# Kernel optimization log

Hardware: AMD Instinct MI355X
Metric: run time of the kernel (lower is better)

## Reference

```python
import jax, jax.numpy as jnp
import numpy as np

B, C, Hd, Wd = 8, 256, 64, 64
NUM_HEAD = 4
RATIO = 0.25
OUT_CH = int(NUM_HEAD * C * RATIO)      # 256
HEAD_DIM = OUT_CH // NUM_HEAD           # 64
EPS = 1e-5


def conv1x1(x, w, b=None):
    # x: [B,Ci,H,W], w: [Co,Ci]
    y = jnp.einsum('bchw,oc->bohw', x, w)
    if b is not None:
        y = y + b[None, :, None, None]
    return y


def setup_inputs() -> dict:
    key = jax.random.key(0)
    ks = jax.random.split(key, 16)
    s = lambda fan: 1.0 / np.sqrt(fan)
    return {
        'key':   jax.random.normal(ks[0], (B, C, Hd, Wd), jnp.float32),
        'query': jax.random.normal(ks[1], (B, C, Hd, Wd), jnp.float32),
        'wq': jax.random.normal(ks[2], (OUT_CH, C), jnp.float32) * s(C),
        'bq': jax.random.normal(ks[3], (OUT_CH,), jnp.float32) * 0.01,
        'wk': jax.random.normal(ks[4], (OUT_CH, C), jnp.float32) * s(C),
        'bk': jax.random.normal(ks[5], (OUT_CH,), jnp.float32) * 0.01,
        'wv': jax.random.normal(ks[6], (OUT_CH, C), jnp.float32) * s(C),
        'bv': jax.random.normal(ks[7], (OUT_CH,), jnp.float32) * 0.01,
        'wW': jax.random.normal(ks[8], (C, HEAD_DIM), jnp.float32) * s(HEAD_DIM),
        'bn_gamma': jnp.ones((C,), jnp.float32),
        'bn_beta': jnp.zeros((C,), jnp.float32),
        'bn_mean': jax.random.normal(ks[9], (C,), jnp.float32) * 0.1,
        'bn_var': jax.random.uniform(ks[10], (C,), jnp.float32, 0.5, 1.5),
        'w3': jax.random.normal(ks[11], (C, 2 * C, 3, 3), jnp.float32) * s(2 * C * 9),
        'b3': jax.random.normal(ks[12], (C,), jnp.float32) * 0.01,
        'w1': jax.random.normal(ks[13], (C, C), jnp.float32) * s(C),
        'b1': jax.random.normal(ks[14], (C,), jnp.float32) * 0.01,
    }


def reference(key, query, wq, bq, wk, bk, wv, bv, wW,
              bn_gamma, bn_beta, bn_mean, bn_var, w3, b3, w1, b1):
    b, c, h, w = query.shape
    q = conv1x1(query, wq, bq).reshape(b, NUM_HEAD, HEAD_DIM, h, w)
    k = conv1x1(key, wk, bk).reshape(b, NUM_HEAD, HEAD_DIM, h, w)
    v = conv1x1(key, wv, bv).reshape(b, NUM_HEAD, HEAD_DIM, h, w)

    att = (q * k).sum(axis=2) / np.sqrt(OUT_CH)          # [b, num_head, h, w]
    sm = jax.nn.softmax(att, axis=1)[:, :, None]         # softmax over heads
    weighted = (v * sm).sum(axis=1)                      # [b, head_dim, h, w]

    # W: 1x1 conv (no bias) + BatchNorm (inference)
    out = conv1x1(weighted, wW)
    inv = bn_gamma / jnp.sqrt(bn_var + EPS)
    out = out * inv[None, :, None, None] + (bn_beta - bn_mean * inv)[None, :, None, None]

    # fuse: ConvBlock (reflect-pad 3x3 conv + ELU) then 1x1 conv
    x = jnp.concatenate([key, out], axis=1)              # [b, 2C, h, w]
    x = jnp.pad(x, ((0, 0), (0, 0), (1, 1), (1, 1)), mode='reflect')
    x = jax.lax.conv_general_dilated(x, w3, (1, 1), 'VALID',
                                     dimension_numbers=('NCHW', 'OIHW', 'NCHW'))
    x = jax.nn.elu(x + b3[None, :, None, None])
    return conv1x1(x, w1, b1)
```

## Files before the change

### kernel.cpp

```cpp
#include <hip/hip_runtime.h>
#include <hip/hip_bf16.h>

typedef unsigned short u16;
typedef unsigned int u32;
typedef short bf16x8 __attribute__((ext_vector_type(8)));
typedef float f32x4 __attribute__((ext_vector_type(4)));

#define NPX 32768

__device__ __forceinline__ u16 f2bf(float f) {
  union { float f; u32 u; } v; v.f = f;
  return (u16)((v.u + 0x7FFFu + ((v.u >> 16) & 1u)) >> 16);
}

__device__ __forceinline__ void gload16(const u16* g, u16* l) {
  __builtin_amdgcn_global_load_lds(
      (const __attribute__((address_space(1))) void*)g,
      (__attribute__((address_space(3))) void*)l, 16, 0, 0);
}


__global__ __launch_bounds__(256) void prep_small(
    const float* __restrict__ wq, const float* __restrict__ wk,
    const float* __restrict__ wv, const float* __restrict__ w1,
    const float* __restrict__ wW, const float* __restrict__ gamma,
    const float* __restrict__ beta, const float* __restrict__ mean,
    const float* __restrict__ var,
    u16* __restrict__ wqb, u16* __restrict__ wkb, u16* __restrict__ wvb,
    u16* __restrict__ w1b, u16* __restrict__ wWpb, float* __restrict__ bWp) {
  int idx = blockIdx.x * 256 + threadIdx.x;
  if (idx < 65536) {
    int o = idx >> 8, c = idx & 255;
    int dst = (c >> 5) * 8192 + o * 32 + ((c >> 3) & 3) * 8 + (c & 7);
    wqb[dst] = f2bf(wq[idx]);
    wkb[dst] = f2bf(wk[idx]);
    wvb[dst] = f2bf(wv[idx]);
    w1b[dst] = f2bf(w1[idx]);
  } else if (idx < 65536 + 16384) {
    int j = idx - 65536;
    int o = j >> 6, c = j & 63;
    float inv = gamma[o] * rsqrtf(var[o] + 1e-5f);
    int dst = (c >> 5) * 8192 + o * 32 + ((c >> 3) & 3) * 8 + (c & 7);
    wWpb[dst] = f2bf(wW[j] * inv);
  } else if (idx < 65536 + 16384 + 256) {
    int o = idx - 65536 - 16384;
    float inv = gamma[o] * rsqrtf(var[o] + 1e-5f);
    bWp[o] = beta[o] - mean[o] * inv;
  }
}

__global__ __launch_bounds__(256) void prep_w3t(const float* __restrict__ w3,
                                                u16* __restrict__ w3c) {
  int idx = blockIdx.x * 256 + threadIdx.x;
  int o = idx >> 9, c = idx & 511;
  int cb = c >> 6, ks = (c >> 5) & 1, lk = (c >> 3) & 3, e = c & 7;
  #pragma unroll
  for (int t = 0; t < 9; ++t)
    w3c[(size_t)(((t * 8 + cb) * 2 + ks) * 256 + o) * 32 + lk * 8 + e] =
        f2bf(w3[idx * 9 + t]);
}

__global__ __launch_bounds__(256, 2) void attn_kernel(
    const float* __restrict__ qsrc, const float* __restrict__ ksrc,
    u16* __restrict__ xcat,
    const u16* __restrict__ wqb, const u16* __restrict__ wkb, const u16* __restrict__ wvb,
    const float* __restrict__ bq, const float* __restrict__ bk, const float* __restrict__ bv,
    const u16* __restrict__ wWpb, const float* __restrict__ bWp) {
  __shared__ __align__(16) char smem[74752];
  u16* aq = (u16*)smem;
  u16* ak = (u16*)(smem + 32768);
  u16* tile = (u16*)(smem + 65536);
  float* att_s = (float*)(smem + 65536);
  u16* wsum = (u16*)(smem + 66560);
  float* wbuf = (float*)smem;
  u16* ob = (u16*)smem;

  int tid = threadIdx.x;
  int lane = tid & 63, wv_ = tid >> 6;
  int lc = lane & 15, lk = lane >> 4;
  int px0 = blockIdx.x * 64;
  int b = px0 >> 12, hw0 = px0 & 4095;

  #pragma unroll
  for (int t = 0; t < 8; ++t) {
    const float* src = (t < 4) ? qsrc : ksrc;
    int cc = t & 3;
    #pragma unroll
    for (int i = 0; i < 4; ++i) {
      int idx = tid + 256 * i;
      int c = idx >> 4, p4 = idx & 15;
      const float4 v = *(const float4*)&src[(size_t)(b * 256 + cc * 64 + c) * 4096 + hw0 + p4 * 4];
      u32 lo = f2bf(v.x) | ((u32)f2bf(v.y) << 16);
      u32 hi = f2bf(v.z) | ((u32)f2bf(v.w) << 16);
      *(uint2*)&tile[c * 72 + p4 * 4] = make_uint2(lo, hi);
    }
    __syncthreads();
    int px = tid >> 2, cq = tid & 3;
    u32 vv[8];
    #pragma unroll
    for (int i = 0; i < 8; ++i) {
      u16 a = tile[(cq * 16 + 2 * i) * 72 + px];
      u16 bb = tile[(cq * 16 + 2 * i + 1) * 72 + px];
      vv[i] = a | ((u32)bb << 16);
    }
    u16* dstl = (t < 4) ? aq : ak;
    int c8 = cc * 8 + cq * 2;
    *(uint4*)(dstl + px * 256 + (c8 ^ (px & 7)) * 8) = make_uint4(vv[0], vv[1], vv[2], vv[3]);
    *(uint4*)(dstl + px * 256 + ((c8 + 1) ^ (px & 7)) * 8) = make_uint4(vv[4], vv[5], vv[6], vv[7]);
    if (t >= 4) {
      u16* dp = xcat + (size_t)(px0 + px) * 512 + cc * 64 + cq * 16;
      *(uint4*)dp = make_uint4(vv[0], vv[1], vv[2], vv[3]);
      *(uint4*)(dp + 8) = make_uint4(vv[4], vv[5], vv[6], vv[7]);
    }
    __syncthreads();
  }

  f32x4 zero4 = {0.f, 0.f, 0.f, 0.f};
  f32x4 accq[4][4], acck[4][4];
  #pragma unroll
  for (int mi = 0; mi < 4; ++mi)
    #pragma unroll
    for (int nj = 0; nj < 4; ++nj) { accq[mi][nj] = zero4; acck[mi][nj] = zero4; }

  #pragma unroll
  for (int kk = 0; kk < 8; ++kk) {
    bf16x8 afq[4], afk[4], bfq[4], bfk[4];
    #pragma unroll
    for (int mi = 0; mi < 4; ++mi) {
      int px = mi * 16 + lc;
      int s = (kk * 4 + lk) ^ (px & 7);
      afq[mi] = *(const bf16x8*)(aq + px * 256 + s * 8);
      afk[mi] = *(const bf16x8*)(ak + px * 256 + s * 8);
    }
    #pragma unroll
    for (int nj = 0; nj < 4; ++nj) {
      int n = wv_ * 64 + nj * 16 + lc;
      bfq[nj] = *(const bf16x8*)(wqb + kk * 8192 + n * 32 + lk * 8);
      bfk[nj] = *(const bf16x8*)(wkb + kk * 8192 + n * 32 + lk * 8);
    }
    #pragma unroll
    for (int mi = 0; mi < 4; ++mi)
      #pragma unroll
      for (int nj = 0; nj < 4; ++nj) {
        accq[mi][nj] = __builtin_amdgcn_mfma_f32_16x16x32_bf16(afq[mi], bfq[nj], accq[mi][nj], 0, 0, 0);
        acck[mi][nj] = __builtin_amdgcn_mfma_f32_16x16x32_bf16(afk[mi], bfk[nj], acck[mi][nj], 0, 0, 0);
      }
  }

  #pragma unroll
  for (int nj = 0; nj < 4; ++nj) {
    float bqv = bq[wv_ * 64 + nj * 16 + lc];
    float bkv = bk[wv_ * 64 + nj * 16 + lc];
    #pragma unroll
    for (int mi = 0; mi < 4; ++mi)
      #pragma unroll
      for (int j = 0; j < 4; ++j) { accq[mi][nj][j] += bqv; acck[mi][nj][j] += bkv; }
  }

  float smx[4][4];
  #pragma unroll
  for (int mi = 0; mi < 4; ++mi)
    #pragma unroll
    for (int j = 0; j < 4; ++j) {
      float p = 0.f;
      #pragma unroll
      for (int nj = 0; nj < 4; ++nj) p += accq[mi][nj][j] * acck[mi][nj][j];
      p += __shfl_xor(p, 1);
      p += __shfl_xor(p, 2);
      p += __shfl_xor(p, 4);
      p += __shfl_xor(p, 8);
      float a = p * 0.0625f;
      smx[mi][j] = a;
      if (lc == 0) att_s[wv_ * 64 + mi * 16 + lk * 4 + j] = a;
    }
  __syncthreads();
  #pragma unroll
  for (int mi = 0; mi < 4; ++mi)
    #pragma unroll
    for (int j = 0; j < 4; ++j) {
      int px = mi * 16 + lk * 4 + j;
      float a0 = att_s[px], a1 = att_s[64 + px], a2 = att_s[128 + px], a3 = att_s[192 + px];
      float mx = fmaxf(fmaxf(a0, a1), fmaxf(a2, a3));
      float e0 = __expf(a0 - mx), e1 = __expf(a1 - mx);
      float e2 = __expf(a2 - mx), e3 = __expf(a3 - mx);
      float den = e0 + e1 + e2 + e3;
      float ew = wv_ == 0 ? e0 : (wv_ == 1 ? e1 : (wv_ == 2 ? e2 : e3));
      smx[mi][j] = ew / den;
    }

  f32x4 accv[4][4];
  #pragma unroll
  for (int mi = 0; mi < 4; ++mi)
    #pragma unroll
    for (int nj = 0; nj < 4; ++nj) accv[mi][nj] = zero4;
  #pragma unroll
  for (int kk = 0; kk < 8; ++kk) {
    bf16x8 af[4], bfr[4];
    #pragma unroll
    for (int mi = 0; mi < 4; ++mi) {
      int px = mi * 16 + lc;
      int s = (kk * 4 + lk) ^ (px & 7);
      af[mi] = *(const bf16x8*)(ak + px * 256 + s * 8);
    }
    #pragma unroll
    for (int nj = 0; nj < 4; ++nj) {
      int n = wv_ * 64 + nj * 16 + lc;
      bfr[nj] = *(const bf16x8*)(wvb + kk * 8192 + n * 32 + lk * 8);
    }
    #pragma unroll
    for (int mi = 0; mi < 4; ++mi)
      #pragma unroll
      for (int nj = 0; nj < 4; ++nj)
        accv[mi][nj] = __builtin_amdgcn_mfma_f32_16x16x32_bf16(af[mi], bfr[nj], accv[mi][nj], 0, 0, 0);
  }
  #pragma unroll
  for (int nj = 0; nj < 4; ++nj) {
    float bvv = bv[wv_ * 64 + nj * 16 + lc];
    #pragma unroll
    for (int mi = 0; mi < 4; ++mi)
      #pragma unroll
      for (int j = 0; j < 4; ++j) accv[mi][nj][j] += bvv;
  }
  __syncthreads();

  #pragma unroll
  for (int mi = 0; mi < 4; ++mi)
    #pragma unroll
    for (int nj = 0; nj < 4; ++nj)
      #pragma unroll
      for (int j = 0; j < 4; ++j) {
        int px = mi * 16 + lk * 4 + j;
        wbuf[(wv_ * 64 + px) * 64 + nj * 16 + lc] = smx[mi][j] * accv[mi][nj][j];
      }
  __syncthreads();

  #pragma unroll
  for (int i = 0; i < 2; ++i) {
    int idx = tid + 256 * i;
    int px = idx >> 3, c = idx & 7;
    float a8[8] = {0.f, 0.f, 0.f, 0.f, 0.f, 0.f, 0.f, 0.f};
    #pragma unroll
    for (int h = 0; h < 4; ++h) {
      const float4* p = (const float4*)(wbuf + ((h * 64 + px) * 64 + c * 8));
      float4 u0 = p[0], u1 = p[1];
      a8[0] += u0.x; a8[1] += u0.y; a8[2] += u0.z; a8[3] += u0.w;
      a8[4] += u1.x; a8[5] += u1.y; a8[6] += u1.z; a8[7] += u1.w;
    }
    u32 p0 = f2bf(a8[0]) | ((u32)f2bf(a8[1]) << 16);
    u32 p1 = f2bf(a8[2]) | ((u32)f2bf(a8[3]) << 16);
    u32 p2 = f2bf(a8[4]) | ((u32)f2bf(a8[5]) << 16);
    u32 p3 = f2bf(a8[6]) | ((u32)f2bf(a8[7]) << 16);
    *(uint4*)(wsum + px * 64 + (c ^ (px & 7)) * 8) = make_uint4(p0, p1, p2, p3);
  }
  __syncthreads();

  f32x4 a4[4][4];
  #pragma unroll
  for (int mi = 0; mi < 4; ++mi)
    #pragma unroll
    for (int nj = 0; nj < 4; ++nj) a4[mi][nj] = zero4;
  #pragma unroll
  for (int kk = 0; kk < 2; ++kk) {
    bf16x8 af[4], bfr[4];
    #pragma unroll
    for (int mi = 0; mi < 4; ++mi) {
      int px = mi * 16 + lc;
      int s = (kk * 4 + lk) ^ (px & 7);
      af[mi] = *(const bf16x8*)(wsum + px * 64 + s * 8);
    }
    #pragma unroll
    for (int nj = 0; nj < 4; ++nj) {
      int n = wv_ * 64 + nj * 16 + lc;
      bfr[nj] = *(const bf16x8*)(wWpb + kk * 8192 + n * 32 + lk * 8);
    }
    #pragma unroll
    for (int mi = 0; mi < 4; ++mi)
      #pragma unroll
      for (int nj = 0; nj < 4; ++nj)
        a4[mi][nj] = __builtin_amdgcn_mfma_f32_16x16x32_bf16(af[mi], bfr[nj], a4[mi][nj], 0, 0, 0);
  }
  #pragma unroll
  for (int nj = 0; nj < 4; ++nj) {
    int o = wv_ * 64 + nj * 16 + lc;
    float bb = bWp[o];
    #pragma unroll
    for (int mi = 0; mi < 4; ++mi)
      #pragma unroll
      for (int j = 0; j < 4; ++j) {
        int px = mi * 16 + lk * 4 + j;
        ob[px * 264 + o] = f2bf(a4[mi][nj][j] + bb);
      }
  }
  __syncthreads();
  #pragma unroll
  for (int i = 0; i < 8; ++i) {
    int idx = tid + 256 * i;
    int px = idx >> 5, c8 = idx & 31;
    *(uint4*)(xcat + (size_t)(px0 + px) * 512 + 256 + c8 * 8) =
        *(const uint4*)(ob + px * 264 + c8 * 8);
  }
}

__global__ __launch_bounds__(512, 2) void conv3_kernel(
    const u16* __restrict__ xcat, const u16* __restrict__ w3c,
    const float* __restrict__ b3, const u16* __restrict__ w1b,
    const float* __restrict__ b1, float* __restrict__ out) {
  extern __shared__ __align__(16) u16 smem[];
  u16* xb0 = smem;
  u16* xb1 = smem + 16896;
  u16* wb0 = smem + 33792;
  u16* wb1 = smem + 50176;

  int tid = threadIdx.x;
  int lane = tid & 63, wave = tid >> 6;
  int lc = lane & 15, lk = lane >> 4;
  int wr = wave >> 2, wc = wave & 3;
  int b = blockIdx.x >> 5, r0 = (blockIdx.x & 31) * 2;

  int gx[4], gxt;
  #pragma unroll
  for (int i = 0; i < 5; ++i) {
    int idx = (i < 4) ? (tid + i * 512) : (2048 + lane);
    int px = idx >> 3, t = idx & 7;
    int row = px / 66;
    int pxr = px - row * 66;
    int h_in = r0 - 1 + row; h_in = h_in < 0 ? 1 : (h_in > 63 ? 62 : h_in);
    int w_in = pxr - 1;      w_in = w_in < 0 ? 1 : (w_in > 63 ? 62 : w_in);
    int g = ((b * 64 + h_in) * 64 + w_in) * 512 + (t ^ (pxr & 7)) * 8;
    if (i < 4) gx[i] = g; else gxt = g;
  }
  int gw[4];
  #pragma unroll
  for (int i = 0; i < 4; ++i) {
    int p = tid + i * 512;
    int j = p ^ ((p >> 3) & 7);
    gw[i] = j * 8;
  }

#define STAGE_X(dst, cb_)                                                      \
  do {                                                                         \
    _Pragma("unroll") for (int i = 0; i < 4; ++i)                              \
        gload16(xcat + gx[i] + (cb_) * 64, (dst) + (size_t)(tid + i * 512) * 8); \
    if (wave == 0) gload16(xcat + gxt + (cb_) * 64, (dst) + (size_t)(2048 + lane) * 8); \
  } while (0)

#define STAGE_W(dst, slab)                                                     \
  do {                                                                         \
    const u16* wsrc = w3c + (size_t)(slab) * 16384;                            \
    _Pragma("unroll") for (int i = 0; i < 4; ++i)                              \
        gload16(wsrc + gw[i], (dst) + (size_t)(tid + i * 512) * 8);            \
  } while (0)

  f32x4 zero4 = {0.f, 0.f, 0.f, 0.f};
  f32x4 acc[4][4];
  #pragma unroll
  for (int mi = 0; mi < 4; ++mi)
    #pragma unroll
    for (int nj = 0; nj < 4; ++nj) acc[mi][nj] = zero4;

  STAGE_X(xb0, 0);
  STAGE_W(wb0, 0);
  __syncthreads();

  for (int cb = 0; cb < 8; ++cb) {
    const u16* xcur = (cb & 1) ? xb1 : xb0;
    #pragma unroll
    for (int tap = 0; tap < 9; ++tap) {
      const u16* wcur = ((cb + tap) & 1) ? wb1 : wb0;
      u16* wnxt = ((cb + tap) & 1) ? wb0 : wb1;
      if (tap < 8) {
        STAGE_W(wnxt, (tap + 1) * 8 + cb);
      } else if (cb < 7) {
        STAGE_W(wnxt, cb + 1);
        STAGE_X((cb & 1) ? xb0 : xb1, cb + 1);
      }
      const int dy = tap / 3, dx = tap % 3;
      #pragma unroll
      for (int ks = 0; ks < 2; ++ks) {
        bf16x8 af[4], bfr[4];
        #pragma unroll
        for (int mi = 0; mi < 4; ++mi) {
          int pp = mi * 16 + lc + dx;
          af[mi] = *(const bf16x8*)(xcur + ((wr + dy) * 66 + pp) * 64 +
                                    (((ks * 4 + lk) ^ (pp & 7)) * 8));
        }
        #pragma unroll
        for (int nj = 0; nj < 4; ++nj) {
          int n = wc * 64 + nj * 16 + lc;
          int j = ks * 1024 + n * 4 + lk;
          int p = j ^ ((j >> 3) & 7);
          bfr[nj] = *(const bf16x8*)(wcur + p * 8);
        }
        __builtin_amdgcn_s_setprio(1);
        #pragma unroll
        for (int mi = 0; mi < 4; ++mi)
          #pragma unroll
          for (int nj = 0; nj < 4; ++nj)
            acc[mi][nj] = __builtin_amdgcn_mfma_f32_16x16x32_bf16(
                af[mi], bfr[nj], acc[mi][nj], 0, 0, 0);
        __builtin_amdgcn_s_setprio(0);
      }
      __syncthreads();
    }
  }
#undef STAGE_X
#undef STAGE_W

  u16* eb = smem;
  #pragma unroll
  for (int nj = 0; nj < 4; ++nj) {
    int o = wc * 64 + nj * 16 + lc;
    float bias = b3[o];
    #pragma unroll
    for (int mi = 0; mi < 4; ++mi)
      #pragma unroll
      for (int j = 0; j < 4; ++j) {
        int p = wr * 64 + mi * 16 + lk * 4 + j;
        float v = acc[mi][nj][j] + bias;
        v = v > 0.f ? v : (__expf(v) - 1.f);
        eb[p * 264 + o] = f2bf(v);
      }
  }
  __syncthreads();

  f32x4 acc2[4][4];
  #pragma unroll
  for (int mi = 0; mi < 4; ++mi)
    #pragma unroll
    for (int nj = 0; nj < 4; ++nj) acc2[mi][nj] = zero4;
  #pragma unroll
  for (int kk = 0; kk < 8; ++kk) {
    bf16x8 af[4], bfr[4];
    #pragma unroll
    for (int mi = 0; mi < 4; ++mi)
      af[mi] = *(const bf16x8*)(eb + (wr * 64 + mi * 16 + lc) * 264 + kk * 32 + lk * 8);
    #pragma unroll
    for (int nj = 0; nj < 4; ++nj)
      bfr[nj] = *(const bf16x8*)(w1b + kk * 8192 + (wc * 64 + nj * 16 + lc) * 32 + lk * 8);
    #pragma unroll
    for (int mi = 0; mi < 4; ++mi)
      #pragma unroll
      for (int nj = 0; nj < 4; ++nj)
        acc2[mi][nj] = __builtin_amdgcn_mfma_f32_16x16x32_bf16(af[mi], bfr[nj], acc2[mi][nj], 0, 0, 0);
  }
  #pragma unroll
  for (int nj = 0; nj < 4; ++nj) {
    int o = wc * 64 + nj * 16 + lc;
    float bias = b1[o];
    #pragma unroll
    for (int mi = 0; mi < 4; ++mi) {
      float4 v;
      v.x = acc2[mi][nj][0] + bias;
      v.y = acc2[mi][nj][1] + bias;
      v.z = acc2[mi][nj][2] + bias;
      v.w = acc2[mi][nj][3] + bias;
      *(float4*)&out[(size_t)(b * 256 + o) * 4096 + (r0 + wr) * 64 + mi * 16 + lk * 4] = v;
    }
  }
}

extern "C" void kernel_launch(void* const* d_in, const int* in_sizes, int n_in,
                              void* d_out, int out_size, void* d_ws, size_t ws_size,
                              hipStream_t stream) {
  const float* key   = (const float*)d_in[0];
  const float* query = (const float*)d_in[1];
  const float* wq    = (const float*)d_in[2];
  const float* bq    = (const float*)d_in[3];
  const float* wk    = (const float*)d_in[4];
  const float* bk    = (const float*)d_in[5];
  const float* wv    = (const float*)d_in[6];
  const float* bv    = (const float*)d_in[7];
  const float* wW    = (const float*)d_in[8];
  const float* gamma = (const float*)d_in[9];
  const float* beta  = (const float*)d_in[10];
  const float* mean  = (const float*)d_in[11];
  const float* var   = (const float*)d_in[12];
  const float* w3    = (const float*)d_in[13];
  const float* b3    = (const float*)d_in[14];
  const float* w1    = (const float*)d_in[15];
  const float* b1    = (const float*)d_in[16];
  float* out = (float*)d_out;

  char* ws = (char*)d_ws;
  u16* xcat  = (u16*)(ws + 16777216);
  u16* w3t   = (u16*)(ws + 67108864);
  u16* wqb   = (u16*)(ws + 69468160);
  u16* wkb   = (u16*)(ws + 69599232);
  u16* wvb   = (u16*)(ws + 69730304);
  u16* w1b   = (u16*)(ws + 69861376);
  u16* wWpb  = (u16*)(ws + 69992448);
  float* bWp = (float*)(ws + 70025216);

  (void)hipFuncSetAttribute((const void*)conv3_kernel,
                            hipFuncAttributeMaxDynamicSharedMemorySize, 133120);

  prep_small<<<321, 256, 0, stream>>>(wq, wk, wv, w1, wW, gamma, beta, mean, var,
                                      wqb, wkb, wvb, w1b, wWpb, bWp);
  prep_w3t<<<512, 256, 0, stream>>>(w3, w3t);
  attn_kernel<<<512, 256, 0, stream>>>(query, key, xcat, wqb, wkb, wvb,
                                       bq, bk, bv, wWpb, bWp);
  conv3_kernel<<<256, 512, 133120, stream>>>(xcat, w3t, b3, w1b, b1, out);
}
```

Before: 118.1 us.

## Shrink conv3 tiles to one output row and 32-channel K slabs for occupancy

The 3x3 conv kernel now has each block compute a single output row instead of two. It uses 32-channel K slabs instead of 64, which shrinks LDS from about 130KB of dynamic memory to about 58KB of static memory and allows more resident blocks per CU with twice as many blocks. The weight repack layout changes to match the new slab size, and block IDs are remapped so that consecutive blocks spread across batches. The trade-off is less reuse per staged tile, twice as many barrier-separated pipeline steps, and more halo reloading of input rows.

After: 134.3 us. +13.7%, slower.

```diff
diff --git a/kernel.cpp b/kernel.cpp
--- a/kernel.cpp
+++ b/kernel.cpp
@@ -53,10 +53,11 @@
                                                 u16* __restrict__ w3c) {
   int idx = blockIdx.x * 256 + threadIdx.x;
   int o = idx >> 9, c = idx & 511;
-  int cb = c >> 6, ks = (c >> 5) & 1, lk = (c >> 3) & 3, e = c & 7;
+  int cb = c >> 5, w = c & 31;
+  int lk = w >> 3, e = w & 7;
   #pragma unroll
   for (int t = 0; t < 9; ++t)
-    w3c[(size_t)(((t * 8 + cb) * 2 + ks) * 256 + o) * 32 + lk * 8 + e] =
+    w3c[(size_t)(t * 16 + cb) * 8192 + o * 32 + lk * 8 + e] =
         f2bf(w3[idx * 9 + t]);
 }
 
@@ -301,60 +302,60 @@
   }
 }
 
-__global__ __launch_bounds__(512, 2) void conv3_kernel(
+__global__ __launch_bounds__(512, 4) void conv3_kernel(
     const u16* __restrict__ xcat, const u16* __restrict__ w3c,
     const float* __restrict__ b3, const u16* __restrict__ w1b,
     const float* __restrict__ b1, float* __restrict__ out) {
-  extern __shared__ __align__(16) u16 smem[];
+  __shared__ __align__(16) u16 smem[29696];
   u16* xb0 = smem;
-  u16* xb1 = smem + 16896;
-  u16* wb0 = smem + 33792;
-  u16* wb1 = smem + 50176;
+  u16* xb1 = smem + 6656;
+  u16* wb0 = smem + 13312;
+  u16* wb1 = smem + 21504;
 
   int tid = threadIdx.x;
   int lane = tid & 63, wave = tid >> 6;
   int lc = lane & 15, lk = lane >> 4;
   int wr = wave >> 2, wc = wave & 3;
-  int b = blockIdx.x >> 5, r0 = (blockIdx.x & 31) * 2;
-
-  int gx[4], gxt;
-  #pragma unroll
-  for (int i = 0; i < 5; ++i) {
-    int idx = (i < 4) ? (tid + i * 512) : (2048 + lane);
-    int px = idx >> 3, t = idx & 7;
-    int row = px / 66;
-    int pxr = px - row * 66;
-    int h_in = r0 - 1 + row; h_in = h_in < 0 ? 1 : (h_in > 63 ? 62 : h_in);
-    int w_in = pxr - 1;      w_in = w_in < 0 ? 1 : (w_in > 63 ? 62 : w_in);
-    int g = ((b * 64 + h_in) * 64 + w_in) * 512 + (t ^ (pxr & 7)) * 8;
-    if (i < 4) gx[i] = g; else gxt = g;
-  }
-  int gw[4];
-  #pragma unroll
-  for (int i = 0; i < 4; ++i) {
-    int p = tid + i * 512;
-    int j = p ^ ((p >> 3) & 7);
-    gw[i] = j * 8;
-  }
-
-#define STAGE_X(dst, cb_)                                                      \
-  do {                                                                         \
-    _Pragma("unroll") for (int i = 0; i < 4; ++i)                              \
-        gload16(xcat + gx[i] + (cb_) * 64, (dst) + (size_t)(tid + i * 512) * 8); \
-    if (wave == 0) gload16(xcat + gxt + (cb_) * 64, (dst) + (size_t)(2048 + lane) * 8); \
+  int sbid = (blockIdx.x & 7) * 64 + (blockIdx.x >> 3);
+  int b = sbid >> 6, r = sbid & 63;
+
+  int gx0, gx1, gx2;
+  #pragma unroll
+  for (int i = 0; i < 3; ++i) {
+    int q = (i == 0) ? tid : (i == 1 ? 512 + tid : 768 + lane);
+    q = q < 792 ? q : 791;
+    int row = q / 264, rem = q - row * 264;
+    int s = rem / 66, px = rem - s * 66;
+    int h_in = r - 1 + row; h_in = h_in < 0 ? 1 : (h_in > 63 ? 62 : h_in);
+    int w_in = px - 1;      w_in = w_in < 0 ? 1 : (w_in > 63 ? 62 : w_in);
+    int g = ((b * 64 + h_in) * 64 + w_in) * 512 + s * 8;
+    if (i == 0) gx0 = g; else if (i == 1) gx1 = g; else gx2 = g;
+  }
+  int gw0, gw1;
+  {
+    int p0 = tid, p1 = tid + 512;
+    gw0 = (p0 ^ ((p0 >> 3) & 7)) * 8;
+    gw1 = (p1 ^ ((p1 >> 3) & 7)) * 8;
+  }
+
+#define STAGE_X(dst, cb_)                                                       \
+  do {                                                                          \
+    gload16(xcat + gx0 + (cb_) * 32, (dst) + (size_t)tid * 8);                  \
+    if (tid < 256) gload16(xcat + gx1 + (cb_) * 32, (dst) + (size_t)(512 + tid) * 8); \
+    if (wave == 0) gload16(xcat + gx2 + (cb_) * 32, (dst) + (size_t)(768 + lane) * 8); \
   } while (0)
 
-#define STAGE_W(dst, slab)                                                     \
-  do {                                                                         \
-    const u16* wsrc = w3c + (size_t)(slab) * 16384;                            \
-    _Pragma("unroll") for (int i = 0; i < 4; ++i)                              \
-        gload16(wsrc + gw[i], (dst) + (size_t)(tid + i * 512) * 8);            \
+#define STAGE_W(dst, slab)                                                      \
+  do {                                                                          \
+    const u16* wsrc = w3c + (size_t)(slab) * 8192;                              \
+    gload16(wsrc + gw0, (dst) + (size_t)tid * 8);                               \
+    gload16(wsrc + gw1, (dst) + (size_t)(tid + 512) * 8);                       \
   } while (0)
 
   f32x4 zero4 = {0.f, 0.f, 0.f, 0.f};
-  f32x4 acc[4][4];
-  #pragma unroll
-  for (int mi = 0; mi < 4; ++mi)
+  f32x4 acc[2][4];
+  #pragma unroll
+  for (int mi = 0; mi < 2; ++mi)
     #pragma unroll
     for (int nj = 0; nj < 4; ++nj) acc[mi][nj] = zero4;
 
@@ -362,44 +363,41 @@
   STAGE_W(wb0, 0);
   __syncthreads();
 
-  for (int cb = 0; cb < 8; ++cb) {
+  for (int cb = 0; cb < 16; ++cb) {
     const u16* xcur = (cb & 1) ? xb1 : xb0;
     #pragma unroll
     for (int tap = 0; tap < 9; ++tap) {
-      const u16* wcur = ((cb + tap) & 1) ? wb1 : wb0;
-      u16* wnxt = ((cb + tap) & 1) ? wb0 : wb1;
+      int par = (cb + tap) & 1;
+      const u16* wcur = par ? wb1 : wb0;
+      u16* wnxt = par ? wb0 : wb1;
       if (tap < 8) {
-        STAGE_W(wnxt, (tap + 1) * 8 + cb);
-      } else if (cb < 7) {
+        STAGE_W(wnxt, (tap + 1) * 16 + cb);
+      } else if (cb < 15) {
         STAGE_W(wnxt, cb + 1);
         STAGE_X((cb & 1) ? xb0 : xb1, cb + 1);
       }
       const int dy = tap / 3, dx = tap % 3;
-      #pragma unroll
-      for (int ks = 0; ks < 2; ++ks) {
-        bf16x8 af[4], bfr[4];
+      bf16x8 af[2], bfr[4];
+      #pragma unroll
+      for (int mi = 0; mi < 2; ++mi) {
+        int pp = wr * 32 + mi * 16 + lc + dx;
+        af[mi] = *(const bf16x8*)(xcur + ((dy * 4 + lk) * 66 + pp) * 8);
+      }
+      #pragma unroll
+      for (int nj = 0; nj < 4; ++nj) {
+        int n = wc * 64 + nj * 16 + lc;
+        int j = n * 4 + lk;
+        int p = j ^ ((j >> 3) & 7);
+        bfr[nj] = *(const bf16x8*)(wcur + p * 8);
+      }
+      __builtin_amdgcn_s_setprio(1);
+      #pragma unroll
+      for (int mi = 0; mi < 2; ++mi)
         #pragma unroll
-        for (int mi = 0; mi < 4; ++mi) {
-          int pp = mi * 16 + lc + dx;
-          af[mi] = *(const bf16x8*)(xcur + ((wr + dy) * 66 + pp) * 64 +
-                                    (((ks * 4 + lk) ^ (pp & 7)) * 8));
-        }
-        #pragma unroll
-        for (int nj = 0; nj < 4; ++nj) {
-          int n = wc * 64 + nj * 16 + lc;
-          int j = ks * 1024 + n * 4 + lk;
-          int p = j ^ ((j >> 3) & 7);
-          bfr[nj] = *(const bf16x8*)(wcur + p * 8);
-        }
-        __builtin_amdgcn_s_setprio(1);
-        #pragma unroll
-        for (int mi = 0; mi < 4; ++mi)
-          #pragma unroll
-          for (int nj = 0; nj < 4; ++nj)
-            acc[mi][nj] = __builtin_amdgcn_mfma_f32_16x16x32_bf16(
-                af[mi], bfr[nj], acc[mi][nj], 0, 0, 0);
-        __builtin_amdgcn_s_setprio(0);
-      }
+        for (int nj = 0; nj < 4; ++nj)
+          acc[mi][nj] = __builtin_amdgcn_mfma_f32_16x16x32_bf16(
+              af[mi], bfr[nj], acc[mi][nj], 0, 0, 0);
+      __builtin_amdgcn_s_setprio(0);
       __syncthreads();
     }
   }
@@ -412,33 +410,33 @@
     int o = wc * 64 + nj * 16 + lc;
     float bias = b3[o];
     #pragma unroll
-    for (int mi = 0; mi < 4; ++mi)
+    for (int mi = 0; mi < 2; ++mi)
       #pragma unroll
       for (int j = 0; j < 4; ++j) {
-        int p = wr * 64 + mi * 16 + lk * 4 + j;
+        int p = wr * 32 + mi * 16 + lk * 4 + j;
         float v = acc[mi][nj][j] + bias;
         v = v > 0.f ? v : (__expf(v) - 1.f);
-        eb[p * 264 + o] = f2bf(v);
-      }
-  }
-  __syncthreads();
-
-  f32x4 acc2[4][4];
-  #pragma unroll
-  for (int mi = 0; mi < 4; ++mi)
+        eb[p * 260 + o] = f2bf(v);
+      }
+  }
+  __syncthreads();
+
+  f32x4 acc2[2][4];
+  #pragma unroll
+  for (int mi = 0; mi < 2; ++mi)
     #pragma unroll
     for (int nj = 0; nj < 4; ++nj) acc2[mi][nj] = zero4;
   #pragma unroll
   for (int kk = 0; kk < 8; ++kk) {
-    bf16x8 af[4], bfr[4];
-    #pragma unroll
-    for (int mi = 0; mi < 4; ++mi)
-      af[mi] = *(const bf16x8*)(eb + (wr * 64 + mi * 16 + lc) * 264 + kk * 32 + lk * 8);
+    bf16x8 af[2], bfr[4];
+    #pragma unroll
+    for (int mi = 0; mi < 2; ++mi)
+      af[mi] = *(const bf16x8*)(eb + (wr * 32 + mi * 16 + lc) * 260 + kk * 32 + lk * 8);
     #pragma unroll
     for (int nj = 0; nj < 4; ++nj)
       bfr[nj] = *(const bf16x8*)(w1b + kk * 8192 + (wc * 64 + nj * 16 + lc) * 32 + lk * 8);
     #pragma unroll
-    for (int mi = 0; mi < 4; ++mi)
+    for (int mi = 0; mi < 2; ++mi)
       #pragma unroll
       for (int nj = 0; nj < 4; ++nj)
         acc2[mi][nj] = __builtin_amdgcn_mfma_f32_16x16x32_bf16(af[mi], bfr[nj], acc2[mi][nj], 0, 0, 0);
@@ -448,13 +446,13 @@
     int o = wc * 64 + nj * 16 + lc;
     float bias = b1[o];
     #pragma unroll
-    for (int mi = 0; mi < 4; ++mi) {
+    for (int mi = 0; mi < 2; ++mi) {
       float4 v;
       v.x = acc2[mi][nj][0] + bias;
       v.y = acc2[mi][nj][1] + bias;
       v.z = acc2[mi][nj][2] + bias;
       v.w = acc2[mi][nj][3] + bias;
-      *(float4*)&out[(size_t)(b * 256 + o) * 4096 + (r0 + wr) * 64 + mi * 16 + lk * 4] = v;
+      *(float4*)&out[(size_t)(b * 256 + o) * 4096 + r * 64 + wr * 32 + mi * 16 + lk * 4] = v;
     }
   }
 }
@@ -491,13 +489,10 @@
   u16* wWpb  = (u16*)(ws + 69992448);
   float* bWp = (float*)(ws + 70025216);
 
-  (void)hipFuncSetAttribute((const void*)conv3_kernel,
-                            hipFuncAttributeMaxDynamicSharedMemorySize, 133120);
-
   prep_small<<<321, 256, 0, stream>>>(wq, wk, wv, w1, wW, gamma, beta, mean, var,
                                       wqb, wkb, wvb, w1b, wWpb, bWp);
   prep_w3t<<<512, 256, 0, stream>>>(w3, w3t);
   attn_kernel<<<512, 256, 0, stream>>>(query, key, xcat, wqb, wkb, wvb,
                                        bq, bk, bv, wWpb, bWp);
-  conv3_kernel<<<256, 512, 133120, stream>>>(xcat, w3t, b3, w1b, b1, out);
-}
+  conv3_kernel<<<512, 512, 0, stream>>>(xcat, w3t, b3, w1b, b1, out);
+}
```

## Restructure conv3 pipeline into 32-channel slabs with 4-deep weight ring buffer

Applied to the files above, without the earlier changes.

The 3x3 conv main loop now walks 16 channel blocks of 32 instead of 8 blocks of 64. Weights stream through a 4-slot ring buffer, prefetched two taps ahead, using explicit vmcnt waits plus barriers in place of full __syncthreads. The input tile layout drops the XOR swizzle in favour of a padded per-subchannel layout, and block indices are remapped across batches. The goal is to cut shared-memory use (133KB to 100KB) and hide global-load latency behind MFMA work, at the cost of fragile hand-counted vmcnt values and possible LDS bank conflicts.

Result: slower. 122.6 us (+3.9%).

```diff
diff --git a/kernel.cpp b/kernel.cpp
--- a/kernel.cpp
+++ b/kernel.cpp
@@ -53,10 +53,11 @@
                                                 u16* __restrict__ w3c) {
   int idx = blockIdx.x * 256 + threadIdx.x;
   int o = idx >> 9, c = idx & 511;
-  int cb = c >> 6, ks = (c >> 5) & 1, lk = (c >> 3) & 3, e = c & 7;
+  int cb = c >> 5;
+  int lk = (c >> 3) & 3, e = c & 7;
   #pragma unroll
   for (int t = 0; t < 9; ++t)
-    w3c[(size_t)(((t * 8 + cb) * 2 + ks) * 256 + o) * 32 + lk * 8 + e] =
+    w3c[(size_t)(cb * 9 + t) * 8192 + o * 32 + lk * 8 + e] =
         f2bf(w3[idx * 9 + t]);
 }
 
@@ -307,48 +308,44 @@
     const float* __restrict__ b1, float* __restrict__ out) {
   extern __shared__ __align__(16) u16 smem[];
   u16* xb0 = smem;
-  u16* xb1 = smem + 16896;
-  u16* wb0 = smem + 33792;
-  u16* wb1 = smem + 50176;
+  u16* xb1 = smem + 8704;
+  u16* wbase = smem + 17408;
 
   int tid = threadIdx.x;
   int lane = tid & 63, wave = tid >> 6;
   int lc = lane & 15, lk = lane >> 4;
   int wr = wave >> 2, wc = wave & 3;
-  int b = blockIdx.x >> 5, r0 = (blockIdx.x & 31) * 2;
-
-  int gx[4], gxt;
-  #pragma unroll
-  for (int i = 0; i < 5; ++i) {
-    int idx = (i < 4) ? (tid + i * 512) : (2048 + lane);
-    int px = idx >> 3, t = idx & 7;
-    int row = px / 66;
-    int pxr = px - row * 66;
+  int sbid = (blockIdx.x & 7) * 32 + (blockIdx.x >> 3);
+  int b = sbid >> 5, r0 = (sbid & 31) * 2;
+
+  int gx0, gx1, gx2;
+  #pragma unroll
+  for (int i = 0; i < 3; ++i) {
+    int c = (i == 0) ? tid : (i == 1 ? tid + 512 : 1024 + lane);
+    int row = c / 272, rem = c - row * 272;
+    int s = rem / 68, px = rem - s * 68;
+    px = px < 66 ? px : 65;
     int h_in = r0 - 1 + row; h_in = h_in < 0 ? 1 : (h_in > 63 ? 62 : h_in);
-    int w_in = pxr - 1;      w_in = w_in < 0 ? 1 : (w_in > 63 ? 62 : w_in);
-    int g = ((b * 64 + h_in) * 64 + w_in) * 512 + (t ^ (pxr & 7)) * 8;
-    if (i < 4) gx[i] = g; else gxt = g;
-  }
-  int gw[4];
-  #pragma unroll
-  for (int i = 0; i < 4; ++i) {
-    int p = tid + i * 512;
-    int j = p ^ ((p >> 3) & 7);
-    gw[i] = j * 8;
-  }
-
-#define STAGE_X(dst, cb_)                                                      \
-  do {                                                                         \
-    _Pragma("unroll") for (int i = 0; i < 4; ++i)                              \
-        gload16(xcat + gx[i] + (cb_) * 64, (dst) + (size_t)(tid + i * 512) * 8); \
-    if (wave == 0) gload16(xcat + gxt + (cb_) * 64, (dst) + (size_t)(2048 + lane) * 8); \
+    int w_in = px - 1;       w_in = w_in < 0 ? 1 : (w_in > 63 ? 62 : w_in);
+    int g = ((b * 64 + h_in) * 64 + w_in) * 512 + s * 8;
+    if (i == 0) gx0 = g; else if (i == 1) gx1 = g; else gx2 = g;
+  }
+  int gw0 = (tid ^ ((tid >> 3) & 7)) * 8;
+  int p1_ = tid + 512;
+  int gw1 = (p1_ ^ ((p1_ >> 3) & 7)) * 8;
+
+#define STAGE_W(dst, slab)                                                      \
+  do {                                                                          \
+    const u16* ws_ = w3c + (size_t)(slab) * 8192;                               \
+    gload16(ws_ + gw0, (dst) + (size_t)tid * 8);                                \
+    gload16(ws_ + gw1, (dst) + (size_t)(tid + 512) * 8);                        \
   } while (0)
 
-#define STAGE_W(dst, slab)                                                     \
-  do {                                                                         \
-    const u16* wsrc = w3c + (size_t)(slab) * 16384;                            \
-    _Pragma("unroll") for (int i = 0; i < 4; ++i)                              \
-        gload16(wsrc + gw[i], (dst) + (size_t)(tid + i * 512) * 8);            \
+#define STAGE_X(dst, cb_)                                                       \
+  do {                                                                          \
+    gload16(xcat + gx0 + (cb_) * 32, (dst) + (size_t)tid * 8);                  \
+    gload16(xcat + gx1 + (cb_) * 32, (dst) + (size_t)(tid + 512) * 8);          \
+    if (wave == 0) gload16(xcat + gx2 + (cb_) * 32, (dst) + (size_t)(1024 + lane) * 8); \
   } while (0)
 
   f32x4 zero4 = {0.f, 0.f, 0.f, 0.f};
@@ -358,53 +355,64 @@
     #pragma unroll
     for (int nj = 0; nj < 4; ++nj) acc[mi][nj] = zero4;
 
+#define COMPUTE(TAP, XB, WIDX)                                                  \
+  do {                                                                          \
+    const u16* wcur_ = wbase + (size_t)(WIDX) * 8192;                           \
+    bf16x8 af[4], bfr[4];                                                       \
+    _Pragma("unroll") for (int mi = 0; mi < 4; ++mi)                            \
+      af[mi] = *(const bf16x8*)((XB) +                                          \
+          (size_t)(((wr + (TAP) / 3) * 4 + lk) * 68 + mi * 16 + lc + (TAP) % 3) * 8); \
+    _Pragma("unroll") for (int nj = 0; nj < 4; ++nj) {                          \
+      int j_ = (wc * 64 + nj * 16 + lc) * 4 + lk;                               \
+      bfr[nj] = *(const bf16x8*)(wcur_ + (size_t)(j_ ^ ((j_ >> 3) & 7)) * 8);   \
+    }                                                                           \
+    __builtin_amdgcn_s_setprio(1);                                              \
+    _Pragma("unroll") for (int mi = 0; mi < 4; ++mi)                            \
+      _Pragma("unroll") for (int nj = 0; nj < 4; ++nj)                          \
+        acc[mi][nj] = __builtin_amdgcn_mfma_f32_16x16x32_bf16(                  \
+            af[mi], bfr[nj], acc[mi][nj], 0, 0, 0);                             \
+    __builtin_amdgcn_s_setprio(0);                                              \
+  } while (0)
+
+  STAGE_W(wbase, 0);
+  STAGE_W(wbase + 8192, 1);
   STAGE_X(xb0, 0);
-  STAGE_W(wb0, 0);
-  __syncthreads();
-
-  for (int cb = 0; cb < 8; ++cb) {
+  asm volatile("s_waitcnt vmcnt(0)\n\ts_barrier" ::: "memory");
+
+  for (int cb = 0; cb < 15; ++cb) {
     const u16* xcur = (cb & 1) ? xb1 : xb0;
-    #pragma unroll
-    for (int tap = 0; tap < 9; ++tap) {
-      const u16* wcur = ((cb + tap) & 1) ? wb1 : wb0;
-      u16* wnxt = ((cb + tap) & 1) ? wb0 : wb1;
-      if (tap < 8) {
-        STAGE_W(wnxt, (tap + 1) * 8 + cb);
-      } else if (cb < 7) {
-        STAGE_W(wnxt, cb + 1);
-        STAGE_X((cb & 1) ? xb0 : xb1, cb + 1);
-      }
-      const int dy = tap / 3, dx = tap % 3;
-      #pragma unroll
-      for (int ks = 0; ks < 2; ++ks) {
-        bf16x8 af[4], bfr[4];
-        #pragma unroll
-        for (int mi = 0; mi < 4; ++mi) {
-          int pp = mi * 16 + lc + dx;
-          af[mi] = *(const bf16x8*)(xcur + ((wr + dy) * 66 + pp) * 64 +
-                                    (((ks * 4 + lk) ^ (pp & 7)) * 8));
-        }
-        #pragma unroll
-        for (int nj = 0; nj < 4; ++nj) {
-          int n = wc * 64 + nj * 16 + lc;
-          int j = ks * 1024 + n * 4 + lk;
-          int p = j ^ ((j >> 3) & 7);
-          bfr[nj] = *(const bf16x8*)(wcur + p * 8);
-        }
-        __builtin_amdgcn_s_setprio(1);
-        #pragma unroll
-        for (int mi = 0; mi < 4; ++mi)
-          #pragma unroll
-          for (int nj = 0; nj < 4; ++nj)
-            acc[mi][nj] = __builtin_amdgcn_mfma_f32_16x16x32_bf16(
-                af[mi], bfr[nj], acc[mi][nj], 0, 0, 0);
-        __builtin_amdgcn_s_setprio(0);
-      }
-      __syncthreads();
-    }
-  }
+    u16* xnxt = (cb & 1) ? xb0 : xb1;
+    int c4 = cb & 3;
+    int base = cb * 9;
+#define PH(TAP)                                                                 \
+    STAGE_W(wbase + (size_t)((c4 + (TAP) + 2) & 3) * 8192, base + (TAP) + 2);   \
+    if ((TAP) == 4) STAGE_X(xnxt, cb + 1);                                      \
+    if ((TAP) < 4) {                                                            \
+      asm volatile("s_waitcnt vmcnt(4)\n\ts_barrier" ::: "memory");             \
+    } else if (wave == 0) {                                                     \
+      asm volatile("s_waitcnt vmcnt(7)\n\ts_barrier" ::: "memory");             \
+    } else {                                                                    \
+      asm volatile("s_waitcnt vmcnt(6)\n\ts_barrier" ::: "memory");             \
+    }                                                                           \
+    COMPUTE(TAP, xcur, (c4 + (TAP)) & 3);
+    PH(0) PH(1) PH(2) PH(3) PH(4) PH(5) PH(6) PH(7) PH(8)
+#undef PH
+  }
+  {
+    const u16* xcur = xb1;
+#define PH15(TAP, WN)                                                           \
+    if ((TAP) < 7) STAGE_W(wbase + (size_t)((3 + (TAP) + 2) & 3) * 8192, 137 + (TAP)); \
+    asm volatile("s_waitcnt vmcnt(" #WN ")\n\ts_barrier" ::: "memory");         \
+    COMPUTE(TAP, xcur, (3 + (TAP)) & 3);
+    PH15(0, 4) PH15(1, 4) PH15(2, 4) PH15(3, 4) PH15(4, 4) PH15(5, 4) PH15(6, 4)
+    PH15(7, 2) PH15(8, 0)
+#undef PH15
+  }
+#undef STAGE_W
 #undef STAGE_X
-#undef STAGE_W
+#undef COMPUTE
+
+  __syncthreads();
 
   u16* eb = smem;
   #pragma unroll
@@ -418,7 +426,7 @@
         int p = wr * 64 + mi * 16 + lk * 4 + j;
         float v = acc[mi][nj][j] + bias;
         v = v > 0.f ? v : (__expf(v) - 1.f);
-        eb[p * 264 + o] = f2bf(v);
+        eb[p * 260 + o] = f2bf(v);
       }
   }
   __syncthreads();
@@ -433,7 +441,7 @@
     bf16x8 af[4], bfr[4];
     #pragma unroll
     for (int mi = 0; mi < 4; ++mi)
-      af[mi] = *(const bf16x8*)(eb + (wr * 64 + mi * 16 + lc) * 264 + kk * 32 + lk * 8);
+      af[mi] = *(const bf16x8*)(eb + (size_t)(wr * 64 + mi * 16 + lc) * 260 + kk * 32 + lk * 8);
     #pragma unroll
     for (int nj = 0; nj < 4; ++nj)
       bfr[nj] = *(const bf16x8*)(w1b + kk * 8192 + (wc * 64 + nj * 16 + lc) * 32 + lk * 8);
@@ -492,12 +500,12 @@
   float* bWp = (float*)(ws + 70025216);
 
   (void)hipFuncSetAttribute((const void*)conv3_kernel,
-                            hipFuncAttributeMaxDynamicSharedMemorySize, 133120);
+                            hipFuncAttributeMaxDynamicSharedMemorySize, 100352);
 
   prep_small<<<321, 256, 0, stream>>>(wq, wk, wv, w1, wW, gamma, beta, mean, var,
                                       wqb, wkb, wvb, w1b, wWpb, bWp);
   prep_w3t<<<512, 256, 0, stream>>>(w3, w3t);
   attn_kernel<<<512, 256, 0, stream>>>(query, key, xcat, wqb, wkb, wvb,
                                        bq, bk, bv, wWpb, bWp);
-  conv3_kernel<<<256, 512, 133120, stream>>>(xcat, w3t, b3, w1b, b1, out);
-}
+  conv3_kernel<<<256, 512, 100352, stream>>>(xcat, w3t, b3, w1b, b1, out);
+}
```
